# Kernel optimization log

Measured on AMD Instinct MI355X. Metric: run time of the kernel, lower is better.

Reference implementation:

```python
import jax, jax.numpy as jnp
import numpy as np

HEADS = 16
KEY_SIZE = 64
HEAD_SIZE = 64
D_MODEL = 1024
MASK_BIG = 1e12


def setup_inputs() -> dict:
    key = jax.random.key(0)
    ks = jax.random.split(key, 16)
    B, S, D = 4, 2048, D_MODEL
    qk_dim = HEADS * KEY_SIZE
    out_dim = HEADS * HEAD_SIZE
    s = 0.02
    return {
        'q': jax.random.normal(ks[0], (B, S, D), jnp.float32),
        'k': jax.random.normal(ks[1], (B, S, D), jnp.float32),
        'v': jax.random.normal(ks[2], (B, S, D), jnp.float32),
        'q_mask': jax.random.randint(ks[3], (B, S), 0, 2, jnp.int32),
        'v_mask': jax.random.randint(ks[4], (B, S), 0, 2, jnp.int32),
        'Wq': jax.random.normal(ks[5], (D, qk_dim), jnp.float32) * s,
        'bq': jnp.zeros((qk_dim,), jnp.float32),
        'Wk': jax.random.normal(ks[6], (D, qk_dim), jnp.float32) * s,
        'bk': jnp.zeros((qk_dim,), jnp.float32),
        'Wv': jax.random.normal(ks[7], (D, out_dim), jnp.float32) * s,
        'bv': jnp.zeros((out_dim,), jnp.float32),
        'Wo': jax.random.normal(ks[8], (out_dim, out_dim), jnp.float32) * s,
        'bo': jnp.zeros((out_dim,), jnp.float32),
    }


def reference(q, k, v, q_mask, v_mask, Wq, bq, Wk, bk, Wv, bv, Wo, bo):
    B, Sq, _ = q.shape
    Sk = k.shape[1]
    # projections -> [B, H, S, d]
    qw = (q @ Wq + bq).reshape(B, Sq, HEADS, KEY_SIZE).transpose(0, 2, 1, 3)
    kw = (k @ Wk + bk).reshape(B, Sk, HEADS, KEY_SIZE).transpose(0, 2, 1, 3)
    vw = (v @ Wv + bv).reshape(B, Sk, HEADS, HEAD_SIZE).transpose(0, 2, 1, 3)
    # scaled dot-product scores [B, H, Sq, Sk]
    a = jnp.einsum('bhqd,bhkd->bhqk', qw, kw) / np.sqrt(KEY_SIZE).astype(np.float32)
    # v_mask: additive -inf-like penalty on padded keys (mode=1, axis=-1)
    vm = v_mask.astype(a.dtype)[:, None, None, :]
    a = a - (1.0 - vm) * MASK_BIG
    # a_mask=True: causal mask (mask future positions)
    causal = jnp.tril(jnp.ones((Sq, Sk), a.dtype))
    a = a - (1.0 - causal) * MASK_BIG
    a = jax.nn.softmax(a, axis=-1)
    # attention output [B, Sq, H*head_size]
    o = jnp.einsum('bhqk,bhkd->bhqd', a, vw).transpose(0, 2, 1, 3).reshape(B, Sq, HEADS * HEAD_SIZE)
    o = o @ Wo + bo
    # q_mask: multiplicative zeroing of padded query outputs (mode=0, axis=1)
    o = o * q_mask.astype(o.dtype)[:, :, None]
    return o
```

## Files before the change

kernel.cpp:

```cpp
#include <hip/hip_runtime.h>
#include <hip/hip_bf16.h>

typedef __attribute__((ext_vector_type(8))) short v8s;
typedef __attribute__((ext_vector_type(4))) float v4f;
typedef __attribute__((ext_vector_type(16))) float v16f;
typedef __attribute__((ext_vector_type(4))) unsigned v4u;

#define S_LEN 2048
#define NB 4
#define NH 16
#define LOG2E 1.4426950408889634f
#define CMASK 1443109011456.0f
#define DEFER_THR 11.55f

__device__ __forceinline__ short f2bf(float f) {
    __hip_bfloat16 h = __float2bfloat16(f);
    union { __hip_bfloat16 h; short s; } u; u.h = h; return u.s;
}

__device__ __forceinline__ unsigned cvtpk(float lo, float hi) {
    unsigned r;
    asm("v_cvt_pk_bf16_f32 %0, %1, %2" : "=v"(r) : "v"(lo), "v"(hi));
    return r;
}

__device__ __forceinline__ int swz(int row, int col) {
    return (row * 128 + col) ^ ((row & 7) << 4);
}

__device__ __forceinline__ void async16(void* lds, const void* g) {
    __builtin_amdgcn_global_load_lds(
        (const __attribute__((address_space(1))) unsigned int*)g,
        (__attribute__((address_space(3))) unsigned int*)lds, 16, 0, 0);
}

#define MFMA16(a, b, c) __builtin_amdgcn_mfma_f32_16x16x32_bf16((a), (b), (c), 0, 0, 0)
#define MFMA32(a, b, c) __builtin_amdgcn_mfma_f32_32x32x16_bf16((a), (b), (c), 0, 0, 0)

__global__ __launch_bounds__(256) void convert_all(const float* __restrict__ q,
                                                   const float* __restrict__ k,
                                                   const float* __restrict__ v,
                                                   short* __restrict__ Xq,
                                                   short* __restrict__ Xk,
                                                   short* __restrict__ Xv,
                                                   float* __restrict__ outz) {
    if (blockIdx.y == 3) {
        size_t i = ((size_t)blockIdx.x * 256 + threadIdx.x) * 8;
        float4 z4 = {0.f, 0.f, 0.f, 0.f};
        *(float4*)(outz + i) = z4;
        *(float4*)(outz + i + 4) = z4;
        return;
    }
    const float* in = (blockIdx.y == 0) ? q : (blockIdx.y == 1) ? k : v;
    short* out = (blockIdx.y == 0) ? Xq : (blockIdx.y == 1) ? Xk : Xv;
    size_t i = ((size_t)blockIdx.x * 256 + threadIdx.x) * 8;
    float4 a = *(const float4*)(in + i);
    float4 b = *(const float4*)(in + i + 4);
    v8s o;
    o[0] = f2bf(a.x); o[1] = f2bf(a.y); o[2] = f2bf(a.z); o[3] = f2bf(a.w);
    o[4] = f2bf(b.x); o[5] = f2bf(b.y); o[6] = f2bf(b.z); o[7] = f2bf(b.w);
    *(v8s*)(out + i) = o;
}

__global__ __launch_bounds__(256) void build_pen(const int* __restrict__ vm,
                                                 short* __restrict__ penC) {
    int i = blockIdx.x * 256 + threadIdx.x;
    penC[i] = vm[i] ? (short)0 : f2bf(-CMASK);
}

__global__ __launch_bounds__(256) void compact_qmask(const int* __restrict__ qm,
                                                     int* __restrict__ idx,
                                                     int* __restrict__ nq) {
    const int b = blockIdx.x;
    const int* m = qm + b * S_LEN;
    int* ib = idx + b * S_LEN;
    __shared__ int cnt[256];
    const int t = threadIdx.x;
    int loc[8], c = 0;
#pragma unroll
    for (int i = 0; i < 8; ++i) { int s = t * 8 + i; if (m[s]) loc[c++] = s; }
    cnt[t] = c;
    __syncthreads();
    for (int d = 1; d < 256; d <<= 1) {
        int v = (t >= d) ? cnt[t - d] : 0;
        __syncthreads();
        cnt[t] += v;
        __syncthreads();
    }
    int off = cnt[t] - c;
    for (int i = 0; i < c; ++i) ib[off + i] = loc[i];
    if (t == 255) nq[b] = cnt[255];
}

__global__ __launch_bounds__(256) void transpose_all(const float* __restrict__ Wq,
                                                     const float* __restrict__ Wk,
                                                     const float* __restrict__ Wv,
                                                     const float* __restrict__ Wo,
                                                     short* __restrict__ WTq,
                                                     short* __restrict__ WTk,
                                                     short* __restrict__ WTv,
                                                     short* __restrict__ WTo) {
    const int z = blockIdx.z;
    const float* W = (z == 0) ? Wq : (z == 1) ? Wk : (z == 2) ? Wv : Wo;
    short* WT = (z == 0) ? WTq : (z == 1) ? WTk : (z == 2) ? WTv : WTo;
    __shared__ float tile[32][33];
    int k0 = blockIdx.x * 32, n0 = blockIdx.y * 32;
    int tx = threadIdx.x & 31, ty = threadIdx.x >> 5;
#pragma unroll
    for (int i = 0; i < 4; ++i)
        tile[ty + i * 8][tx] = W[(size_t)(k0 + ty + i * 8) * 1024 + n0 + tx];
    __syncthreads();
#pragma unroll
    for (int i = 0; i < 4; ++i)
        WT[(size_t)(n0 + ty + i * 8) * 1024 + k0 + tx] = f2bf(tile[tx][ty + i * 8]);
}

__global__ __launch_bounds__(256)
void proj_all(const short* __restrict__ Xk, const short* __restrict__ Xv,
              const short* __restrict__ Xq,
              const short* __restrict__ WTk, const short* __restrict__ WTv,
              const short* __restrict__ WTq,
              const float* __restrict__ bk, const float* __restrict__ bv,
              const float* __restrict__ bq,
              const int* __restrict__ idx, const int* __restrict__ nq,
              short* __restrict__ KF, short* __restrict__ VF,
              short* __restrict__ QW) {
    __shared__ short As[128 * 64];
    __shared__ short Bs[128 * 64];
    const int tid = threadIdx.x;
    const int l = tid & 63, w = tid >> 6;
    const int g = l >> 4, ql = l & 15;
    const int z = blockIdx.z;
    const int bid = blockIdx.x;
    const int y = (bid & 7) + 8 * (bid >> 6);
    const int n0 = ((bid >> 3) & 7) * 128;
    const int wr = w >> 1, wc = w & 1;

    int b = 0, m0 = y * 128, m0c = 0, nqv = 0;
    const int* idxb = nullptr;
    if (z == 2) {
        if (y >= 36) return;
        b = y / 9; m0c = (y % 9) * 128;
        nqv = nq[b];
        if (m0c >= nqv) return;
        idxb = idx + b * S_LEN;
    }
    const short* A  = (z == 0) ? Xk : (z == 1) ? Xv : Xq;
    const short* BT = (z == 0) ? WTk : (z == 1) ? WTv : WTq;
    const float* bias = (z == 0) ? bk : (z == 1) ? bv : bq;

    int arow[4];
#pragma unroll
    for (int i = 0; i < 4; ++i) {
        int row = (i * 256 + tid) >> 3;
        if (z == 2) {
            int jc = m0c + row;
            arow[i] = b * S_LEN + idxb[(jc < nqv) ? jc : (nqv - 1)];
        } else {
            arow[i] = m0 + row;
        }
    }
    const int c8 = (((l & 7) ^ (l >> 3))) * 8;

    v4f acc[4][4] = {};

    for (int kt = 0; kt < 16; ++kt) {
        const int kk = kt * 64;
        __syncthreads();
#pragma unroll
        for (int i = 0; i < 4; ++i) {
            int ci = i * 256 + tid;
            async16((char*)As + (size_t)(i * 256 + w * 64) * 16,
                    A + (size_t)arow[i] * 1024 + kk + c8);
            async16((char*)Bs + (size_t)(i * 256 + w * 64) * 16,
                    BT + (size_t)(n0 + (ci >> 3)) * 1024 + kk + c8);
        }
        __syncthreads();
#pragma unroll
        for (int ks = 0; ks < 2; ++ks) {
            v8s af[4], bfr[4];
#pragma unroll
            for (int mt = 0; mt < 4; ++mt)
                af[mt] = *(const v8s*)((char*)As +
                          swz(wr * 64 + mt * 16 + ql, ks * 64 + g * 16));
#pragma unroll
            for (int nt = 0; nt < 4; ++nt)
                bfr[nt] = *(const v8s*)((char*)Bs +
                          swz(wc * 64 + nt * 16 + ql, ks * 64 + g * 16));
#pragma unroll
            for (int mt = 0; mt < 4; ++mt)
#pragma unroll
                for (int nt = 0; nt < 4; ++nt)
                    acc[mt][nt] = MFMA16(af[mt], bfr[nt], acc[mt][nt]);
        }
    }

#pragma unroll
    for (int nt = 0; nt < 4; ++nt) {
        int col = n0 + wc * 64 + nt * 16 + ql;
        float bval = bias[col];
        int hh = col >> 6, dd = col & 63;
#pragma unroll
        for (int mt = 0; mt < 4; ++mt) {
#pragma unroll
            for (int r = 0; r < 4; ++r) {
                int lrow = wr * 64 + mt * 16 + g * 4 + r;
                float vv = acc[mt][nt][r] + bval;
                if (z == 0) {
                    int gm = m0 + lrow;
                    int bb = gm >> 11, ss = gm & 2047;
                    size_t base = (size_t)(bb * NH + hh) * 131072
                                + (size_t)(ss >> 6) * 4096
                                + (dd >> 4) * 1024 + (ss & 63) * 16
                                + ((dd >> 3) & 1) * 8 + (dd & 7);
                    KF[base] = f2bf(vv);
                } else if (z == 1) {
                    int gm = m0 + lrow;
                    int bb = gm >> 11, ss = gm & 2047;
                    int wkp = ss & 63;
                    size_t base = (size_t)(bb * NH + hh) * 131072
                                + (size_t)(ss >> 6) * 4096
                                + (wkp >> 4) * 1024 + dd * 16
                                + ((wkp >> 3) & 1) * 8 + (wkp & 7);
                    VF[base] = f2bf(vv);
                } else {
                    int jc = m0c + lrow;
                    vv *= 0.125f * LOG2E;
                    QW[((size_t)(b * NH + hh) * S_LEN + jc) * 64 + dd] = f2bf(vv);
                }
            }
        }
    }
}

__global__ __launch_bounds__(64)
void attn_kernel(const short* __restrict__ QW, const short* __restrict__ KF,
                 const short* __restrict__ VF, const short* __restrict__ penC,
                 const int* __restrict__ idx, const int* __restrict__ nq,
                 short* __restrict__ O) {
    const int l = threadIdx.x;
    const int lq = l & 31, hi = l >> 5;
    const int bh = blockIdx.x;
    const int chunk = 63 - (int)blockIdx.y;
    const int b = bh >> 4, hd = bh & 15;

    const int nqv = nq[b];
    const int cy = chunk * 32;
    if (cy >= nqv) return;

    const short* Qp = QW + (size_t)bh * S_LEN * 64;
    const short* Kp = KF + (size_t)bh * 131072;
    const short* Vp = VF + (size_t)bh * 131072;
    const short* pp = penC + b * S_LEN;
    const int* idxb = idx + b * S_LEN;

    const int j = cy + lq;
    const int jj = (j < nqv) ? j : (nqv - 1);
    const int q_glob = idxb[jj];
    const int qmin = __builtin_amdgcn_readfirstlane(q_glob);

    int lastj = cy + 31; if (lastj > nqv - 1) lastj = nqv - 1;
    const int NT = (idxb[lastj] >> 6) + 1;

    v8s qf[4];
#pragma unroll
    for (int ks = 0; ks < 4; ++ks)
        qf[ks] = *(const v8s*)(Qp + (size_t)jj * 64 + ks * 16 + hi * 8);
    v8s qf4 = {};
    qf4[0] = hi ? (short)0 : (short)0x3F80;

    v16f accO[2] = {};
    float m_run = -INFINITY, l_run = 0.f;

    auto tile = [&](int kt, bool causal) {
        const int k0 = kt * 64;
        const short* Kt = Kp + (size_t)kt * 4096;
        const short* Vt = Vp + (size_t)kt * 4096;
        short p0 = pp[k0 + lq], p1 = pp[k0 + lq + 32];

        v8s kf0[4], kf1[4];
#pragma unroll
        for (int ks = 0; ks < 4; ++ks) {
            kf0[ks] = *(const v8s*)(Kt + ks * 1024 + lq * 16 + hi * 8);
            kf1[ks] = *(const v8s*)(Kt + ks * 1024 + (lq + 32) * 16 + hi * 8);
        }
        v16f acc0 = {}, acc1 = {};
        __builtin_amdgcn_s_setprio(1);
#pragma unroll
        for (int ks = 0; ks < 4; ++ks) {
            acc0 = MFMA32(kf0[ks], qf[ks], acc0);
            acc1 = MFMA32(kf1[ks], qf[ks], acc1);
        }
        v8s k4a = {}, k4b = {};
        k4a[0] = hi ? (short)0 : p0;
        k4b[0] = hi ? (short)0 : p1;
        acc0 = MFMA32(k4a, qf4, acc0);
        acc1 = MFMA32(k4b, qf4, acc1);
        __builtin_amdgcn_s_setprio(0);

        float s[32];
#pragma unroll
        for (int jn = 0; jn < 16; ++jn) { s[jn] = acc0[jn]; s[16 + jn] = acc1[jn]; }
        if (causal) {
#pragma unroll
            for (int t = 0; t < 2; ++t)
#pragma unroll
                for (int jn = 0; jn < 16; ++jn) {
                    int kp = k0 + t * 32 + (jn & 3) + 8 * (jn >> 2) + 4 * hi;
                    if (kp > q_glob) s[t * 16 + jn] -= CMASK;
                }
        }
        float t8[8];
#pragma unroll
        for (int i = 0; i < 8; ++i)
            t8[i] = fmaxf(fmaxf(s[i], s[i + 8]), fmaxf(s[i + 16], s[i + 24]));
#pragma unroll
        for (int i = 0; i < 4; ++i) t8[i] = fmaxf(t8[i], t8[i + 4]);
        float tmax = fmaxf(fmaxf(t8[0], t8[1]), fmaxf(t8[2], t8[3]));
        tmax = fmaxf(tmax, __shfl_xor(tmax, 32, 64));

        if (__any(tmax > m_run + DEFER_THR)) {
            float mnew = fmaxf(m_run, tmax);
            float scale = exp2f(m_run - mnew);
            m_run = mnew;
            l_run *= scale;
#pragma unroll
            for (int jn = 0; jn < 16; ++jn) {
                float sc = __shfl(scale, (jn & 3) + 8 * (jn >> 2) + 4 * hi, 64);
                accO[0][jn] *= sc;
                accO[1][jn] *= sc;
            }
        }
#pragma unroll
        for (int i = 0; i < 32; ++i) s[i] = exp2f(s[i] - m_run);
        float u8[8];
#pragma unroll
        for (int i = 0; i < 8; ++i)
            u8[i] = (s[i] + s[i + 8]) + (s[i + 16] + s[i + 24]);
#pragma unroll
        for (int i = 0; i < 4; ++i) u8[i] += u8[i + 4];
        float psum = (u8[0] + u8[1]) + (u8[2] + u8[3]);
        psum += __shfl_xor(psum, 32, 64);
        l_run += psum;

        v8s vf0[4], vf1[4];
#pragma unroll
        for (int ks = 0; ks < 4; ++ks) {
            vf0[ks] = *(const v8s*)(Vt + ks * 1024 + lq * 16 + hi * 8);
            vf1[ks] = *(const v8s*)(Vt + ks * 1024 + (lq + 32) * 16 + hi * 8);
        }

        v8s PA[4];
#pragma unroll
        for (int t = 0; t < 2; ++t)
#pragma unroll
            for (int sf = 0; sf < 2; ++sf) {
                int base = t * 16 + sf * 8;
                unsigned x0 = cvtpk(s[base + 0], s[base + 1]);
                unsigned x1 = cvtpk(s[base + 2], s[base + 3]);
                unsigned y0 = cvtpk(s[base + 4], s[base + 5]);
                unsigned y1 = cvtpk(s[base + 6], s[base + 7]);
                asm volatile("v_permlane32_swap_b32 %0, %1" : "+v"(x0), "+v"(y0));
                asm volatile("v_permlane32_swap_b32 %0, %1" : "+v"(x1), "+v"(y1));
                v4u wv; wv[0] = x0; wv[1] = x1; wv[2] = y0; wv[3] = y1;
                union { v4u u; v8s s8; } cvt; cvt.u = wv;
                PA[t * 2 + sf] = cvt.s8;
            }

        __builtin_amdgcn_s_setprio(1);
#pragma unroll
        for (int ks = 0; ks < 4; ++ks) {
            accO[0] = MFMA32(PA[ks], vf0[ks], accO[0]);
            accO[1] = MFMA32(PA[ks], vf1[ks], accO[1]);
        }
        __builtin_amdgcn_s_setprio(0);
    };

    for (int kt = 0; kt < NT; ++kt)
        tile(kt, kt * 64 + 63 > qmin);

    int kt = NT;
    while (kt < 32 && __any(m_run < -1e11f)) {
        tile(kt, true);
        ++kt;
    }

    float inv = 1.0f / l_run;
#pragma unroll
    for (int jn = 0; jn < 16; ++jn) {
        int rowq = (jn & 3) + 8 * (jn >> 2) + 4 * hi;
        float iv = __shfl(inv, rowq, 64);
        int jrow = cy + rowq;
        if (jrow < nqv) {
            size_t base = (size_t)(b * S_LEN + jrow) * 1024 + hd * 64 + lq;
            O[base]      = f2bf(accO[0][jn] * iv);
            O[base + 32] = f2bf(accO[1][jn] * iv);
        }
    }
}

__global__ __launch_bounds__(256)
void out_gemm_c(const short* __restrict__ A, const short* __restrict__ BT,
                const float* __restrict__ bias, const int* __restrict__ idx,
                const int* __restrict__ nq, float* __restrict__ out) {
    __shared__ short As[128 * 64];
    __shared__ short Bs[128 * 64];
    const int tid = threadIdx.x;
    const int l = tid & 63, w = tid >> 6;
    const int g = l >> 4, ql = l & 15;
    const int bid = blockIdx.x;
    const int y = (bid & 7) + 8 * (bid >> 6);
    if (y >= 36) return;
    const int n0 = ((bid >> 3) & 7) * 128;
    const int b = y / 9;
    const int m0c = (y % 9) * 128;
    const int nqv = nq[b];
    if (m0c >= nqv) return;
    const int* idxb = idx + b * S_LEN;
    const int wr = w >> 1, wc = w & 1;
    const int c8 = (((l & 7) ^ (l >> 3))) * 8;

    v4f acc[4][4] = {};

    for (int kt = 0; kt < 16; ++kt) {
        const int kk = kt * 64;
        __syncthreads();
#pragma unroll
        for (int i = 0; i < 4; ++i) {
            int ci = i * 256 + tid;
            int row = ci >> 3;
            async16((char*)As + (size_t)(i * 256 + w * 64) * 16,
                    A + (size_t)(b * S_LEN + m0c + row) * 1024 + kk + c8);
            async16((char*)Bs + (size_t)(i * 256 + w * 64) * 16,
                    BT + (size_t)(n0 + row) * 1024 + kk + c8);
        }
        __syncthreads();
#pragma unroll
        for (int ks = 0; ks < 2; ++ks) {
            v8s af[4], bfr[4];
#pragma unroll
            for (int mt = 0; mt < 4; ++mt)
                af[mt] = *(const v8s*)((char*)As +
                          swz(wr * 64 + mt * 16 + ql, ks * 64 + g * 16));
#pragma unroll
            for (int nt = 0; nt < 4; ++nt)
                bfr[nt] = *(const v8s*)((char*)Bs +
                          swz(wc * 64 + nt * 16 + ql, ks * 64 + g * 16));
#pragma unroll
            for (int mt = 0; mt < 4; ++mt)
#pragma unroll
                for (int nt = 0; nt < 4; ++nt)
                    acc[mt][nt] = MFMA16(af[mt], bfr[nt], acc[mt][nt]);
        }
    }

#pragma unroll
    for (int nt = 0; nt < 4; ++nt) {
        int col = n0 + wc * 64 + nt * 16 + ql;
        float bval = bias[col];
#pragma unroll
        for (int mt = 0; mt < 4; ++mt) {
#pragma unroll
            for (int r = 0; r < 4; ++r) {
                int jc = m0c + wr * 64 + mt * 16 + g * 4 + r;
                if (jc < nqv) {
                    int orig = idxb[jc];
                    out[(size_t)(b * S_LEN + orig) * 1024 + col] =
                        acc[mt][nt][r] + bval;
                }
            }
        }
    }
}

extern "C" void kernel_launch(void* const* d_in, const int* in_sizes, int n_in,
                              void* d_out, int out_size, void* d_ws, size_t ws_size,
                              hipStream_t stream) {
    (void)in_sizes; (void)n_in; (void)out_size; (void)ws_size;
    const float* q  = (const float*)d_in[0];
    const float* k  = (const float*)d_in[1];
    const float* v  = (const float*)d_in[2];
    const int* qmask = (const int*)d_in[3];
    const int* vmask = (const int*)d_in[4];
    const float* Wq = (const float*)d_in[5];
    const float* bq = (const float*)d_in[6];
    const float* Wk = (const float*)d_in[7];
    const float* bk = (const float*)d_in[8];
    const float* Wv = (const float*)d_in[9];
    const float* bv = (const float*)d_in[10];
    const float* Wo = (const float*)d_in[11];
    const float* bo = (const float*)d_in[12];
    float* out = (float*)d_out;

    char* ws = (char*)d_ws;
    const size_t MB = 1024 * 1024;
    short* Xq  = (short*)(ws + 0 * MB);
    short* Xk  = (short*)(ws + 16 * MB);
    short* Xv  = (short*)(ws + 32 * MB);
    short* WTq = (short*)(ws + 48 * MB);
    short* WTk = (short*)(ws + 50 * MB);
    short* WTv = (short*)(ws + 52 * MB);
    short* WTo = (short*)(ws + 54 * MB);
    short* QW  = (short*)(ws + 56 * MB);
    short* KF  = (short*)(ws + 72 * MB);
    short* VFb = (short*)(ws + 88 * MB);
    short* Ob  = (short*)(ws + 104 * MB);
    short* penC = (short*)(ws + 120 * MB);
    int* idxB  = (int*)(ws + 121 * MB);
    int* nqB   = (int*)(ws + 122 * MB);

    convert_all<<<dim3(4096, 4), 256, 0, stream>>>(q, k, v, Xq, Xk, Xv, out);
    transpose_all<<<dim3(32, 32, 4), 256, 0, stream>>>(Wq, Wk, Wv, Wo,
                                                       WTq, WTk, WTv, WTo);
    build_pen<<<32, 256, 0, stream>>>(vmask, penC);
    compact_qmask<<<NB, 256, 0, stream>>>(qmask, idxB, nqB);

    proj_all<<<dim3(512, 1, 3), 256, 0, stream>>>(Xk, Xv, Xq, WTk, WTv, WTq,
                                                  bk, bv, bq, idxB, nqB,
                                                  KF, VFb, QW);
    attn_kernel<<<dim3(64, 64), 64, 0, stream>>>(QW, KF, VFb, penC, idxB, nqB, Ob);
    out_gemm_c<<<320, 256, 0, stream>>>(Ob, WTo, bo, idxB, nqB, out);
}
```

Baseline: 227.3 us.

## Double-buffer LDS tiles in projection and output GEMMs to overlap loads

Both the QKV projection GEMM and the output GEMM now keep two shared-memory buffers for the A and B tiles. The async global-to-LDS copies for the next k-tile are issued before computing on the current one, and a partial vmcnt wait lets those loads stay in flight during the MFMA work. This targets the memory latency that was fully exposed by the load, sync, compute pattern. In exchange, LDS use per block doubles from 32 KB to 64 KB, which may lower occupancy, and correctness depends on the hand-written waitcnt and barrier ordering.

```diff
diff --git a/kernel.cpp b/kernel.cpp
--- a/kernel.cpp
+++ b/kernel.cpp
@@ -125,8 +125,8 @@
               const int* __restrict__ idx, const int* __restrict__ nq,
               short* __restrict__ KF, short* __restrict__ VF,
               short* __restrict__ QW) {
-    __shared__ short As[128 * 64];
-    __shared__ short Bs[128 * 64];
+    __shared__ short As[2][128 * 64];
+    __shared__ short Bs[2][128 * 64];
     const int tid = threadIdx.x;
     const int l = tid & 63, w = tid >> 6;
     const int g = l >> 4, ql = l & 15;
@@ -164,28 +164,43 @@
 
     v4f acc[4][4] = {};
 
-    for (int kt = 0; kt < 16; ++kt) {
+    auto stage = [&](int kt, int buf) {
         const int kk = kt * 64;
-        __syncthreads();
 #pragma unroll
         for (int i = 0; i < 4; ++i) {
             int ci = i * 256 + tid;
-            async16((char*)As + (size_t)(i * 256 + w * 64) * 16,
+            async16((char*)As[buf] + (size_t)(i * 256 + w * 64) * 16,
                     A + (size_t)arow[i] * 1024 + kk + c8);
-            async16((char*)Bs + (size_t)(i * 256 + w * 64) * 16,
+            async16((char*)Bs[buf] + (size_t)(i * 256 + w * 64) * 16,
                     BT + (size_t)(n0 + (ci >> 3)) * 1024 + kk + c8);
         }
-        __syncthreads();
+    };
+
+    stage(0, 0);
+    for (int kt = 0; kt < 16; ++kt) {
+        __builtin_amdgcn_s_barrier();
+        __builtin_amdgcn_sched_barrier(0);
+        if (kt + 1 < 16) {
+            stage(kt + 1, (kt + 1) & 1);
+            asm volatile("s_waitcnt vmcnt(8)" ::: "memory");
+        } else {
+            asm volatile("s_waitcnt vmcnt(0)" ::: "memory");
+        }
+        __builtin_amdgcn_sched_barrier(0);
+        __builtin_amdgcn_s_barrier();
+        __builtin_amdgcn_sched_barrier(0);
+        const short* Ab = As[kt & 1];
+        const short* Bb = Bs[kt & 1];
 #pragma unroll
         for (int ks = 0; ks < 2; ++ks) {
             v8s af[4], bfr[4];
 #pragma unroll
             for (int mt = 0; mt < 4; ++mt)
-                af[mt] = *(const v8s*)((char*)As +
+                af[mt] = *(const v8s*)((char*)Ab +
                           swz(wr * 64 + mt * 16 + ql, ks * 64 + g * 16));
 #pragma unroll
             for (int nt = 0; nt < 4; ++nt)
-                bfr[nt] = *(const v8s*)((char*)Bs +
+                bfr[nt] = *(const v8s*)((char*)Bb +
                           swz(wc * 64 + nt * 16 + ql, ks * 64 + g * 16));
 #pragma unroll
             for (int mt = 0; mt < 4; ++mt)
@@ -403,8 +418,8 @@
 void out_gemm_c(const short* __restrict__ A, const short* __restrict__ BT,
                 const float* __restrict__ bias, const int* __restrict__ idx,
                 const int* __restrict__ nq, float* __restrict__ out) {
-    __shared__ short As[128 * 64];
-    __shared__ short Bs[128 * 64];
+    __shared__ short As[2][128 * 64];
+    __shared__ short Bs[2][128 * 64];
     const int tid = threadIdx.x;
     const int l = tid & 63, w = tid >> 6;
     const int g = l >> 4, ql = l & 15;
@@ -422,29 +437,44 @@
 
     v4f acc[4][4] = {};
 
-    for (int kt = 0; kt < 16; ++kt) {
+    auto stage = [&](int kt, int buf) {
         const int kk = kt * 64;
-        __syncthreads();
 #pragma unroll
         for (int i = 0; i < 4; ++i) {
             int ci = i * 256 + tid;
             int row = ci >> 3;
-            async16((char*)As + (size_t)(i * 256 + w * 64) * 16,
+            async16((char*)As[buf] + (size_t)(i * 256 + w * 64) * 16,
                     A + (size_t)(b * S_LEN + m0c + row) * 1024 + kk + c8);
-            async16((char*)Bs + (size_t)(i * 256 + w * 64) * 16,
+            async16((char*)Bs[buf] + (size_t)(i * 256 + w * 64) * 16,
                     BT + (size_t)(n0 + row) * 1024 + kk + c8);
         }
-        __syncthreads();
+    };
+
+    stage(0, 0);
+    for (int kt = 0; kt < 16; ++kt) {
+        __builtin_amdgcn_s_barrier();
+        __builtin_amdgcn_sched_barrier(0);
+        if (kt + 1 < 16) {
+            stage(kt + 1, (kt + 1) & 1);
+            asm volatile("s_waitcnt vmcnt(8)" ::: "memory");
+        } else {
+            asm volatile("s_waitcnt vmcnt(0)" ::: "memory");
+        }
+        __builtin_amdgcn_sched_barrier(0);
+        __builtin_amdgcn_s_barrier();
+        __builtin_amdgcn_sched_barrier(0);
+        const short* Ab = As[kt & 1];
+        const short* Bb = Bs[kt & 1];
 #pragma unroll
         for (int ks = 0; ks < 2; ++ks) {
             v8s af[4], bfr[4];
 #pragma unroll
             for (int mt = 0; mt < 4; ++mt)
-                af[mt] = *(const v8s*)((char*)As +
+                af[mt] = *(const v8s*)((char*)Ab +
                           swz(wr * 64 + mt * 16 + ql, ks * 64 + g * 16));
 #pragma unroll
             for (int nt = 0; nt < 4; ++nt)
-                bfr[nt] = *(const v8s*)((char*)Bs +
+                bfr[nt] = *(const v8s*)((char*)Bb +
                           swz(wc * 64 + nt * 16 + ql, ks * 64 + g * 16));
 #pragma unroll
             for (int mt = 0; mt < 4; ++mt)
```

After: 219.9 us, median of 2. -3.2%, faster.
